# Kernel tuning notes

Measured on AMD Instinct MI355X. Metric: run time of the kernel, lower is better.

The kernel has to match this reference:

```python
import jax, jax.numpy as jnp
import numpy as np

N, K, D_IN, D_OUT = 50000, 32, 128, 128
TEMPERATURE = 1.0


def setup_inputs() -> dict:
    key = jax.random.key(0)
    k1, k2, k3 = jax.random.split(key, 3)
    feat = jax.random.normal(k1, (N, D_IN), dtype=jnp.float32)
    # Glorot-like scale so pairwise distances stay in a reasonable softmax range
    weight = jax.random.normal(k2, (D_IN, D_OUT), dtype=jnp.float32) / np.sqrt(D_IN)
    bias = jnp.zeros((D_OUT,), dtype=jnp.float32)
    # norm='none' -> unit edge weights; fixed-degree-k graph -> topk returns all k neighbors
    top_k_weights = jnp.ones((N, K), dtype=jnp.float32)
    top_k_idx = jax.random.randint(k3, (N, K), 0, N, dtype=jnp.int64)
    return {"feat": feat, "weight": weight, "bias": bias,
            "top_k_weights": top_k_weights, "top_k_idx": top_k_idx}


def reference(feat, weight, bias, top_k_weights, top_k_idx):
    # Linear projection (self.weight): [n, d_out]
    h = feat @ weight
    # Gather top-k neighbor embeddings: [n, k, d]
    fk = h[top_k_idx]
    mask = top_k_idx == -1                      # [n, k] missing-neighbor mask
    w = jnp.where(mask, 0.0, top_k_weights)     # zero out missing weights

    # Pairwise Euclidean distances among each node's k neighbors: [n, k, k]
    # ||a-b|| = sqrt(|a|^2 + |b|^2 - 2 a.b); avoids materializing [n,k,k,d]
    sq = jnp.sum(fk * fk, axis=-1)                          # [n, k]
    gram = jnp.einsum('nkd,nmd->nkm', fk, fk)               # [n, k, k]
    d2 = sq[:, :, None] + sq[:, None, :] - 2.0 * gram
    d2 = jnp.maximum(d2, 0.0)
    dist = jnp.sqrt(jnp.where(d2 > 0.0, d2, 1.0))
    dist = jnp.where(d2 > 0.0, dist, 0.0)                   # zero for identical pts / -1 idx
    # zero entries for missing pairs (matches partial_distance_matrix semantics)
    pair_mask = mask[:, :, None] | mask[:, None, :]
    dist = jnp.where(pair_mask, 0.0, dist)

    # Weighted sum of distances over neighbors (medoid cost): [n, k]
    dagg = jnp.einsum('nm,nkm->nk', w, dist)
    big = jnp.finfo(dist.dtype).max
    dagg = jnp.where(mask | ~jnp.isfinite(dagg), big, dagg)

    # Soft medoid weights
    r = jax.nn.softmax(-dagg / TEMPERATURE, axis=-1)
    # with_weight_correction=True
    r = r * w
    r = r / jnp.sum(r, axis=-1, keepdims=True)
    r = jnp.where(mask, 0.0, r)

    # spmm over the reliable adjacency: [n, d_out]
    out = jnp.einsum('nk,nkd->nd', r, fk)
    return out + bias
```

## Files before the change

kernel.cpp:

```cpp
#include <hip/hip_runtime.h>
#include <math.h>


typedef __attribute__((ext_vector_type(4)))  _Float16 half4v;
typedef __attribute__((ext_vector_type(8)))  _Float16 half8;
typedef __attribute__((ext_vector_type(16))) float    f32x16;

#define NK   32
#define DIM  128
#define FKS  136

__global__ __launch_bounds__(256) void prep(const float* __restrict__ W,
                                            _Float16* __restrict__ WT) {
    int t  = blockIdx.x * 256 + threadIdx.x;
    int nn = t >> 7, k = t & 127;
    WT[t] = (_Float16)W[k * 128 + nn];
}

__global__ __launch_bounds__(256) void gemm128(
    const float* __restrict__ A, const _Float16* __restrict__ WT,
    _Float16* __restrict__ Hq, int n)
{
    const int wave = threadIdx.x >> 6;
    const int lane = threadIdx.x & 63;
    const int l31  = lane & 31;
    const int hf   = lane >> 5;

    const int row  = blockIdx.x * 128 + wave * 32 + l31;
    const int rowc = row < n ? row : n - 1;

    f32x16 acc[4];
#pragma unroll
    for (int t = 0; t < 4; ++t)
#pragma unroll
        for (int i = 0; i < 16; ++i) acc[t][i] = 0.0f;

    const float* ap = A + (size_t)rowc * 128 + 8 * hf;
#pragma unroll
    for (int s = 0; s < 8; ++s) {
        float4 b0 = *reinterpret_cast<const float4*>(ap + 16 * s);
        float4 b1 = *reinterpret_cast<const float4*>(ap + 16 * s + 4);
        half8 bf;
        bf[0] = (_Float16)b0.x; bf[1] = (_Float16)b0.y;
        bf[2] = (_Float16)b0.z; bf[3] = (_Float16)b0.w;
        bf[4] = (_Float16)b1.x; bf[5] = (_Float16)b1.y;
        bf[6] = (_Float16)b1.z; bf[7] = (_Float16)b1.w;
#pragma unroll
        for (int t = 0; t < 4; ++t) {
            half8 af = *reinterpret_cast<const half8*>(
                WT + (size_t)(l31 + 32 * t) * 128 + 16 * s + 8 * hf);
            acc[t] = __builtin_amdgcn_mfma_f32_32x32x16_f16(af, bf, acc[t], 0, 0, 0);
        }
    }

    if (row < n) {
        _Float16* hp = Hq + (size_t)row * 128;
#pragma unroll
        for (int t = 0; t < 4; ++t)
#pragma unroll
            for (int g = 0; g < 4; ++g) {
                half4v hv;
#pragma unroll
                for (int q = 0; q < 4; ++q) hv[q] = (_Float16)acc[t][4 * g + q];
                *reinterpret_cast<half4v*>(hp + 32 * t + 8 * g + 4 * hf) = hv;
            }
    }
}

__global__ __launch_bounds__(128, 4) void softk(
    const _Float16* __restrict__ hq, const float* __restrict__ bias,
    const float* __restrict__ tkw, const int* __restrict__ idx,
    float* __restrict__ out, int n)
{
    __shared__ __align__(16) _Float16 fkRM[2][NK][FKS];

    const int wave = threadIdx.x >> 6;
    const int lane = threadIdx.x & 63;
    int node = blockIdx.x * 2 + wave;
    if (node >= n) node = n - 1;

    const int l31 = lane & 31;
    const int hf  = lane >> 5;

    int id_l = 0, mk_l = 0; float w_l = 0.0f;
    if (lane < NK) {
        int id = idx[(size_t)node * NK + lane];
        mk_l = (id < 0) ? 1 : 0;
        id_l = mk_l ? 0 : id;
        w_l  = mk_l ? 0.0f : tkw[(size_t)node * NK + lane];
    }
    const int idr = __shfl(id_l, l31, 64);

    const half8* bp = reinterpret_cast<const half8*>(hq + (size_t)idr * DIM);
    half8 frag[8];
#pragma unroll
    for (int s = 0; s < 8; ++s) frag[s] = bp[2 * s + hf];

    f32x16 acc;
#pragma unroll
    for (int i = 0; i < 16; ++i) acc[i] = 0.0f;
#pragma unroll
    for (int s = 0; s < 8; ++s)
        acc = __builtin_amdgcn_mfma_f32_32x32x16_f16(frag[s], frag[s], acc, 0, 0, 0);

#pragma unroll
    for (int s = 0; s < 8; ++s)
        *reinterpret_cast<half8*>(&fkRM[wave][l31][16 * s + 8 * hf]) = frag[s];

    float dval = acc[0];
#pragma unroll
    for (int reg = 0; reg < 16; ++reg) {
        int rD = (reg & 3) + 8 * (reg >> 2) + 4 * hf;
        if (rD == l31) dval = acc[reg];
    }
    const bool own = (((l31 >> 2) & 1) == hf);
    float oth = __shfl_xor(dval, 32, 64);
    float sqc = own ? dval : oth;

    float wc  = __shfl(w_l,  l31, 64);
    int   mkc = __shfl(mk_l, l31, 64);

    const int pbase = (lane & 32) + ((lane & 32) >> 3);
    float part = 0.0f;
#pragma unroll
    for (int reg = 0; reg < 16; ++reg) {
        const int c = (reg & 3) + 8 * (reg >> 2);
        float sqr = __shfl(sqc, pbase + c, 64);
        float wr  = __shfl(wc,  pbase + c, 64);
        float d2  = fmaf(-2.0f, acc[reg], sqr + sqc);
        part = fmaf(wr, __builtin_amdgcn_sqrtf(fmaxf(d2, 0.0f)), part);
    }
    float sA = part + __shfl_xor(part, 32, 64);
    if (mkc || !(sA < 3.4028235e38f)) sA = 3.4028235e38f;

    float x  = -sA;
    float mx = x;
#pragma unroll
    for (int o = 16; o > 0; o >>= 1) mx = fmaxf(mx, __shfl_xor(mx, o, 32));
    float e  = __expf(x - mx);
    float se = e;
#pragma unroll
    for (int o = 16; o > 0; o >>= 1) se += __shfl_xor(se, o, 32);
    float r = e * __builtin_amdgcn_rcpf(se);
    r *= wc;
    float sr = r;
#pragma unroll
    for (int o = 16; o > 0; o >>= 1) sr += __shfl_xor(sr, o, 32);
    r = r * __builtin_amdgcn_rcpf(sr);
    if (mkc) r = 0.0f;

    half8 a0, a1;
#pragma unroll
    for (int j = 0; j < 8; ++j) {
        a0[j] = (_Float16)__shfl(r, 8 * hf + j, 64);
        a1[j] = (_Float16)__shfl(r, 16 + 8 * hf + j, 64);
    }
    float ov[4];
#pragma unroll
    for (int t = 0; t < 4; ++t) {
        half8 b0, b1;
#pragma unroll
        for (int j = 0; j < 8; ++j) {
            b0[j] = fkRM[wave][8 * hf + j][32 * t + l31];
            b1[j] = fkRM[wave][16 + 8 * hf + j][32 * t + l31];
        }
        f32x16 oacc;
#pragma unroll
        for (int i = 0; i < 16; ++i) oacc[i] = 0.0f;
        oacc = __builtin_amdgcn_mfma_f32_32x32x16_f16(a0, b0, oacc, 0, 0, 0);
        oacc = __builtin_amdgcn_mfma_f32_32x32x16_f16(a1, b1, oacc, 0, 0, 0);
        ov[t] = oacc[0];
    }
#pragma unroll
    for (int u = 0; u < 2; ++u) {
        int t = 2 * hf + u;
        int d = 32 * t + l31;
        out[(size_t)node * DIM + d] = ov[t] + bias[d];
    }
}

extern "C" void kernel_launch(void* const* d_in, const int* in_sizes, int n_in,
                              void* d_out, int out_size, void* d_ws, size_t ws_size,
                              hipStream_t stream) {
    const float* feat = (const float*)d_in[0];
    const float* W    = (const float*)d_in[1];
    const float* bias = (const float*)d_in[2];
    const float* tkw  = (const float*)d_in[3];
    const int*   idx  = (const int*)d_in[4];
    float* out = (float*)d_out;

    const int n = in_sizes[0] / DIM;
    _Float16* hq = (_Float16*)d_ws;
    _Float16* wt = hq + (size_t)n * DIM;

    prep<<<64, 256, 0, stream>>>(W, wt);
    gemm128<<<(n + 127) / 128, 256, 0, stream>>>(feat, wt, hq, n);
    softk<<<(n + 1) / 2, 128, 0, stream>>>(hq, bias, tkw, idx, out, n);
}
```

Measured before the change: 167.0 us.

## Fold norms into MFMA, drop LDS staging, re-gather neighbors for output

Squared norms are folded into the Gram accumulator through an extra MFMA with split-fp16 augmented operands, which removes the per-element shuffles for sq and weights. The LDS staging of neighbor rows is removed. The final weighted sum now re-reads each neighbor row from global/L2 with scalar FMAs instead of the LDS+MFMA reduction. Blocks grow to 4 waves. Together this cuts shuffles and LDS traffic but adds 32 re-gathers per node, a d2 threshold change, and fp16 split precision in the norms.

Result: slower. 217.4 us (+30.2%).

```diff
diff --git a/kernel.cpp b/kernel.cpp
--- a/kernel.cpp
+++ b/kernel.cpp
@@ -2,13 +2,13 @@
 #include <math.h>
 
 
+typedef __attribute__((ext_vector_type(2)))  _Float16 half2v;
 typedef __attribute__((ext_vector_type(4)))  _Float16 half4v;
 typedef __attribute__((ext_vector_type(8)))  _Float16 half8;
 typedef __attribute__((ext_vector_type(16))) float    f32x16;
 
 #define NK   32
 #define DIM  128
-#define FKS  136
 
 __global__ __launch_bounds__(256) void prep(const float* __restrict__ W,
                                             _Float16* __restrict__ WT) {
@@ -67,29 +67,26 @@
     }
 }
 
-__global__ __launch_bounds__(128, 4) void softk(
+__global__ __launch_bounds__(256, 4) void softk(
     const _Float16* __restrict__ hq, const float* __restrict__ bias,
     const float* __restrict__ tkw, const int* __restrict__ idx,
     float* __restrict__ out, int n)
 {
-    __shared__ __align__(16) _Float16 fkRM[2][NK][FKS];
-
     const int wave = threadIdx.x >> 6;
     const int lane = threadIdx.x & 63;
-    int node = blockIdx.x * 2 + wave;
+    int node = blockIdx.x * 4 + wave;
     if (node >= n) node = n - 1;
 
     const int l31 = lane & 31;
     const int hf  = lane >> 5;
 
-    int id_l = 0, mk_l = 0; float w_l = 0.0f;
-    if (lane < NK) {
-        int id = idx[(size_t)node * NK + lane];
-        mk_l = (id < 0) ? 1 : 0;
-        id_l = mk_l ? 0 : id;
-        w_l  = mk_l ? 0.0f : tkw[(size_t)node * NK + lane];
-    }
-    const int idr = __shfl(id_l, l31, 64);
+    const int*   idp = idx + (size_t)node * NK;
+    const float* twp = tkw + (size_t)node * NK;
+
+    const int vid = idp[l31];
+    const int mkc = (vid < 0) ? 1 : 0;
+    const int idr = mkc ? 0 : vid;
+    const float wc = mkc ? 0.0f : twp[l31];
 
     const half8* bp = reinterpret_cast<const half8*>(hq + (size_t)idr * DIM);
     half8 frag[8];
@@ -103,10 +100,6 @@
     for (int s = 0; s < 8; ++s)
         acc = __builtin_amdgcn_mfma_f32_32x32x16_f16(frag[s], frag[s], acc, 0, 0, 0);
 
-#pragma unroll
-    for (int s = 0; s < 8; ++s)
-        *reinterpret_cast<half8*>(&fkRM[wave][l31][16 * s + 8 * hf]) = frag[s];
-
     float dval = acc[0];
 #pragma unroll
     for (int reg = 0; reg < 16; ++reg) {
@@ -115,20 +108,34 @@
     }
     const bool own = (((l31 >> 2) & 1) == hf);
     float oth = __shfl_xor(dval, 32, 64);
-    float sqc = own ? dval : oth;
+    float sq  = own ? dval : oth;
 
-    float wc  = __shfl(w_l,  l31, 64);
-    int   mkc = __shfl(mk_l, l31, 64);
+    {
+        _Float16 shi = (_Float16)sq;
+        _Float16 slo = (_Float16)(sq - (float)shi);
+        _Float16 nh  = (_Float16)(-0.5f * (float)shi);
+        _Float16 nl  = (_Float16)(-0.5f * (float)slo);
+        _Float16 z   = (_Float16)0.0f, one = (_Float16)1.0f;
+        half8 aext = {z, z, z, z, z, z, z, z};
+        half8 bext = {z, z, z, z, z, z, z, z};
+        if (hf == 0) {
+            aext[0] = nh;  aext[1] = nl;  aext[2] = one; aext[3] = one;
+            bext[0] = one; bext[1] = one; bext[2] = nh;  bext[3] = nl;
+        }
+        acc = __builtin_amdgcn_mfma_f32_32x32x16_f16(aext, bext, acc, 0, 0, 0);
+    }
 
-    const int pbase = (lane & 32) + ((lane & 32) >> 3);
     float part = 0.0f;
 #pragma unroll
     for (int reg = 0; reg < 16; ++reg) {
         const int c = (reg & 3) + 8 * (reg >> 2);
-        float sqr = __shfl(sqc, pbase + c, 64);
-        float wr  = __shfl(wc,  pbase + c, 64);
-        float d2  = fmaf(-2.0f, acc[reg], sqr + sqc);
-        part = fmaf(wr, __builtin_amdgcn_sqrtf(fmaxf(d2, 0.0f)), part);
+        int   ia = idp[c],     ib = idp[c + 4];
+        float wa = (ia < 0) ? 0.0f : twp[c];
+        float wb = (ib < 0) ? 0.0f : twp[c + 4];
+        float wr = hf ? wb : wa;
+        float d2 = fmaxf(-(acc[reg] + acc[reg]), 0.0f);
+        float ds = (d2 > 1e-4f) ? __builtin_amdgcn_sqrtf(d2) : 0.0f;
+        part = fmaf(wr, ds, part);
     }
     float sA = part + __shfl_xor(part, 32, 64);
     if (mkc || !(sA < 3.4028235e38f)) sA = 3.4028235e38f;
@@ -149,34 +156,21 @@
     r = r * __builtin_amdgcn_rcpf(sr);
     if (mkc) r = 0.0f;
 
-    half8 a0, a1;
+    float o0 = 0.0f, o1 = 0.0f;
 #pragma unroll
-    for (int j = 0; j < 8; ++j) {
-        a0[j] = (_Float16)__shfl(r, 8 * hf + j, 64);
-        a1[j] = (_Float16)__shfl(r, 16 + 8 * hf + j, 64);
+    for (int k = 0; k < NK; ++k) {
+        int idk = idp[k];
+        idk = idk < 0 ? 0 : idk;
+        float rk = __shfl(r, k, 64);
+        half2v hv = *reinterpret_cast<const half2v*>(
+            hq + (size_t)idk * DIM + 2 * lane);
+        o0 = fmaf(rk, (float)hv[0], o0);
+        o1 = fmaf(rk, (float)hv[1], o1);
     }
-    float ov[4];
-#pragma unroll
-    for (int t = 0; t < 4; ++t) {
-        half8 b0, b1;
-#pragma unroll
-        for (int j = 0; j < 8; ++j) {
-            b0[j] = fkRM[wave][8 * hf + j][32 * t + l31];
-            b1[j] = fkRM[wave][16 + 8 * hf + j][32 * t + l31];
-        }
-        f32x16 oacc;
-#pragma unroll
-        for (int i = 0; i < 16; ++i) oacc[i] = 0.0f;
-        oacc = __builtin_amdgcn_mfma_f32_32x32x16_f16(a0, b0, oacc, 0, 0, 0);
-        oacc = __builtin_amdgcn_mfma_f32_32x32x16_f16(a1, b1, oacc, 0, 0, 0);
-        ov[t] = oacc[0];
-    }
-#pragma unroll
-    for (int u = 0; u < 2; ++u) {
-        int t = 2 * hf + u;
-        int d = 32 * t + l31;
-        out[(size_t)node * DIM + d] = ov[t] + bias[d];
-    }
+    const int d0 = 2 * lane;
+    float2 bv = *reinterpret_cast<const float2*>(bias + d0);
+    float2 ov = { o0 + bv.x, o1 + bv.y };
+    *reinterpret_cast<float2*>(out + (size_t)node * DIM + d0) = ov;
 }
 
 extern "C" void kernel_launch(void* const* d_in, const int* in_sizes, int n_in,
@@ -195,5 +189,5 @@
 
     prep<<<64, 256, 0, stream>>>(W, wt);
     gemm128<<<(n + 127) / 128, 256, 0, stream>>>(feat, wt, hq, n);
-    softk<<<(n + 1) / 2, 128, 0, stream>>>(hq, bias, tkw, idx, out, n);
+    softk<<<(n + 3) / 4, 256, 0, stream>>>(hq, bias, tkw, idx, out, n);
 }
```
